# Optimization experiments

Measured on AMD Instinct MI355X. Metric: run time of the kernel, lower is better.

## Reference

```python
import jax, jax.numpy as jnp
import numpy as np
import math

B, S, D, H = 8, 256, 4096, 16
HD = D // H  # 256 == S, so the module's transposed mask application is exactly elementwise


def setup_inputs() -> dict:
    key = jax.random.key(0)
    ks = jax.random.split(key, 12)
    sc = 1.0 / math.sqrt(D)
    inp = {
        "q": jax.random.normal(ks[0], (B, S, D), dtype=jnp.float32),
        "k": jax.random.normal(ks[1], (B, S, D), dtype=jnp.float32),
        "v": jax.random.normal(ks[2], (B, S, D), dtype=jnp.float32),
        "mask": jax.random.randint(ks[3], (B, S), 0, 2),
        "Wq": jax.random.normal(ks[4], (D, D), dtype=jnp.float32) * sc,
        "bq": jnp.zeros((D,), dtype=jnp.float32),
        "Wk": jax.random.normal(ks[5], (D, D), dtype=jnp.float32) * sc,
        "bk": jnp.zeros((D,), dtype=jnp.float32),
        "Wv": jax.random.normal(ks[6], (D, D), dtype=jnp.float32) * sc,
        "bv": jnp.zeros((D,), dtype=jnp.float32),
        "Wo": jax.random.normal(ks[7], (D, D), dtype=jnp.float32) * sc,
        "bo": jnp.zeros((D,), dtype=jnp.float32),
    }
    return inp


def reference(q, k, v, mask, Wq, bq, Wk, bk, Wv, bv, Wo, bo):
    def proj(x, W, b):
        # nn.Linear: x @ W.T + b ; then [B,S,H,HD] -> [B,H,S,HD]
        return (x @ W.T + b).reshape(B, S, H, HD).transpose(0, 2, 1, 3)

    qh = proj(q, Wq, bq)
    kh = proj(k, Wk, bk)
    vh = proj(v, Wv, bv)

    # torch: attn_mask = (mask==0).view(bs,1,1,-1).repeat(1,H,HD,1) -> [B,H,HD,S]
    # then where(attn_mask, 0, q) against q of shape [B,H,S,HD] (elementwise since HD==S)
    am = jnp.broadcast_to((mask == 0)[:, None, None, :], (B, H, HD, S))
    qh = jnp.where(am, 0.0, qh)
    kh = jnp.where(am, 0.0, kh)

    scale = 1.0 / math.sqrt(HD)
    scores = jnp.einsum('bhqd,bhkd->bhqk', qh, kh) * scale
    w = jax.nn.softmax(scores, axis=-1)
    out = jnp.einsum('bhqk,bhkd->bhqd', w, vh)
    out = out.transpose(0, 2, 1, 3).reshape(B, S, D)
    out = out * (D ** -0.5)
    return out @ Wo.T + bo
```

## Files before the change

### kernel.cpp

```cpp
#include <hip/hip_runtime.h>


typedef _Float16 f16;
typedef f16 f16x8 __attribute__((ext_vector_type(8)));
typedef float f32x4 __attribute__((ext_vector_type(4)));

__device__ __forceinline__ void g2lds(const f16* g, f16* l) {
  __builtin_amdgcn_global_load_lds((const __attribute__((address_space(1))) void*)g,
                                   (__attribute__((address_space(3))) void*)l, 16, 0, 0);
}

__global__ __launch_bounds__(256) void cvt_kernel(const float* __restrict__ in,
                                                  f16* __restrict__ out, int n) {
  int i = (blockIdx.x * 256 + threadIdx.x) * 8;
  if (i >= n) return;
  float4 a = *(const float4*)(in + i);
  float4 b = *(const float4*)(in + i + 4);
  f16x8 o;
  o[0] = (f16)a.x; o[1] = (f16)a.y; o[2] = (f16)a.z; o[3] = (f16)a.w;
  o[4] = (f16)b.x; o[5] = (f16)b.y; o[6] = (f16)b.z; o[7] = (f16)b.w;
  *(f16x8*)(out + i) = o;
}

template<int EPI>
__global__ __launch_bounds__(512, 2) void gemm_dp(
    const f16* __restrict__ A, const f16* __restrict__ B,
    const float* __restrict__ bias, const int* __restrict__ mask,
    void* __restrict__ out, int M, int N, int K)
{
  __shared__ __align__(16) f16 lds[3 * 24576];
  const int tid = threadIdx.x;
  const int lane = tid & 63, wid = tid >> 6;
  const int wm = wid >> 2, wn = wid & 3;
  const int ln = lane & 15, lh = lane >> 4;
  const int bm = blockIdx.y, bn = blockIdx.x;

  const size_t Abase = (size_t)bm * 128 * K;
  const size_t Bbase = (size_t)bn * 256 * K;

  const int sr = tid >> 3;
  const int ss = (tid & 7) ^ (sr & 7);

  const int NT = K >> 6;

  f16* p0 = &lds[0];
  f16* p1 = &lds[24576];
  f16* p2 = &lds[2 * 24576];

#define STAGE(t_, bo_, part)                                                    \
  do {                                                                          \
    const int kt_ = (t_) << 6;                                                  \
    if ((part) == 0) {                                                          \
      g2lds(A + Abase + (size_t)sr * K + kt_ + ss * 8,         (bo_) + tid * 8);  \
      g2lds(B + Bbase + (size_t)sr * K + kt_ + ss * 8,         (bo_) + 8192 + tid * 8); \
      g2lds(B + Bbase + (size_t)(64 + sr) * K + kt_ + ss * 8,  (bo_) + 8192 + (512 + tid) * 8); \
    } else {                                                                    \
      g2lds(A + Abase + (size_t)(64 + sr) * K + kt_ + ss * 8,  (bo_) + (512 + tid) * 8); \
      g2lds(B + Bbase + (size_t)(128 + sr) * K + kt_ + ss * 8, (bo_) + 8192 + (1024 + tid) * 8); \
      g2lds(B + Bbase + (size_t)(192 + sr) * K + kt_ + ss * 8, (bo_) + 8192 + (1536 + tid) * 8); \
    }                                                                           \
  } while (0)

  const int lx = ln & 7;
  const int arow = (wm * 64 + ln) * 64;
  const int brow = (wn * 64 + ln) * 64;

#define LOADFRAGS(fa, fb, buf, ks)                                              \
  do {                                                                          \
    const f16* bA_ = (buf);                                                     \
    const f16* bB_ = (buf) + 8192;                                              \
    const int so_ = (((ks) * 4 + lh) ^ lx) * 8;                                 \
    _Pragma("unroll")                                                           \
    for (int mf = 0; mf < 4; ++mf)                                              \
      fa[mf] = *(const f16x8*)&bA_[arow + mf * 1024 + so_];                     \
    _Pragma("unroll")                                                           \
    for (int nf = 0; nf < 4; ++nf)                                              \
      fb[nf] = *(const f16x8*)&bB_[brow + nf * 1024 + so_];                     \
  } while (0)

#define MFMA16(fa, fb)                                                          \
  do {                                                                          \
    __builtin_amdgcn_s_setprio(1);                                              \
    _Pragma("unroll")                                                           \
    for (int mf = 0; mf < 4; ++mf)                                              \
      _Pragma("unroll")                                                         \
      for (int nf = 0; nf < 4; ++nf)                                            \
        acc[mf][nf] = __builtin_amdgcn_mfma_f32_16x16x32_f16(fa[mf], fb[nf],    \
                                                             acc[mf][nf], 0, 0, 0); \
    __builtin_amdgcn_s_setprio(0);                                              \
  } while (0)

  f32x4 acc[4][4] = {};
  f16x8 ca[4], cb[4], na[4], nb[4];

  STAGE(0, p0, 0); STAGE(0, p0, 1);
  STAGE(1, p1, 0); STAGE(1, p1, 1);
  asm volatile("s_waitcnt vmcnt(6)" ::: "memory");
  __builtin_amdgcn_s_barrier();
  asm volatile("" ::: "memory");
  LOADFRAGS(ca, cb, p0, 0);

  for (int t = 0; t < NT; ++t) {
    LOADFRAGS(na, nb, p0, 1);
    if (t + 2 < NT) { STAGE(t + 2, p2, 0); STAGE(t + 2, p2, 1); }
    MFMA16(ca, cb);

    if (t + 1 < NT) {
      if (t + 2 < NT) {
        asm volatile("s_waitcnt vmcnt(6)" ::: "memory");
      } else {
        asm volatile("s_waitcnt vmcnt(0)" ::: "memory");
      }
      __builtin_amdgcn_s_barrier();
      asm volatile("" ::: "memory");
      LOADFRAGS(ca, cb, p1, 0);
      MFMA16(na, nb);
      asm volatile("" ::: "memory");
      __builtin_amdgcn_s_barrier();
      asm volatile("" ::: "memory");
      f16* tp = p0; p0 = p1; p1 = p2; p2 = tp;
    } else {
      MFMA16(na, nb);
    }
  }
#undef STAGE
#undef LOADFRAGS
#undef MFMA16

#pragma unroll
  for (int mf = 0; mf < 4; ++mf)
#pragma unroll
    for (int nf = 0; nf < 4; ++nf)
#pragma unroll
      for (int i = 0; i < 4; ++i) {
        int R = bm * 128 + wm * 64 + mf * 16 + lh * 4 + i;
        int C = bn * 256 + wn * 64 + nf * 16 + ln;
        float v = acc[mf][nf][i];
        if (EPI == 0) {
          v += bias[C];
          v = mask[(R >> 8) * 256 + (C & 255)] ? v : 0.0f;
          ((f16*)out)[(size_t)((R >> 8) * 16 + (C >> 8)) * 65536 +
                      (size_t)(R & 255) * 256 + (C & 255)] = (f16)v;
        } else if (EPI == 1) {
          v += bias[R];
          ((f16*)out)[(size_t)(C >> 8) * 1048576 + (size_t)R * 256 + (C & 255)] = (f16)v;
        } else {
          v += bias[C];
          ((float*)out)[(size_t)R * N + C] = v;
        }
      }
}

__global__ __launch_bounds__(256) void attn_kernel(
    const f16* __restrict__ Q, const f16* __restrict__ Kt,
    const f16* __restrict__ Vt, f16* __restrict__ aout)
{
  __shared__ __align__(16) f16 tile[64 * 256];
  __shared__ __align__(16) f16 pbuf[64 * 256];
  const int tid = threadIdx.x;
  const int lane = tid & 63, w = tid >> 6;
  const int ln = lane & 15, lh = lane >> 4;
  const int bh = blockIdx.x >> 2, rb = blockIdx.x & 3;
  const int b = bh >> 4, h = bh & 15;
  const size_t hb = (size_t)bh * 65536;

  const int strow = tid >> 5;
  const int stsl  = (tid & 31) ^ (strow & 7);

  f16x8 aq[8];
  {
    const f16* qp = Q + hb + (size_t)(rb * 64 + w * 16 + ln) * 256;
#pragma unroll
    for (int ks = 0; ks < 8; ++ks)
      aq[ks] = *(const f16x8*)(qp + ks * 32 + lh * 8);
  }

  f32x4 sacc[16] = {};

  for (int kt = 0; kt < 4; ++kt) {
#pragma unroll
    for (int c = 0; c < 8; ++c) {
      int L = c * 256 + tid;
      int row = c * 8 + strow;
      g2lds(Kt + hb + (size_t)(kt * 64 + row) * 256 + stsl * 8, &tile[L * 8]);
    }
    __syncthreads();
#pragma unroll
    for (int nf = 0; nf < 4; ++nf) {
      f16x8 bf[8];
#pragma unroll
      for (int ks = 0; ks < 8; ++ks) {
        int r = nf * 16 + ln;
        int sl = (ks * 4 + lh) ^ (r & 7);
        bf[ks] = *(const f16x8*)&tile[r * 256 + sl * 8];
      }
#pragma unroll
      for (int ks = 0; ks < 8; ++ks)
        sacc[kt * 4 + nf] = __builtin_amdgcn_mfma_f32_16x16x32_f16(
            aq[ks], bf[ks], sacc[kt * 4 + nf], 0, 0, 0);
    }
    __syncthreads();
  }

  const float SC = 1.0f / 16.0f;
  float mrow[4] = {-1e30f, -1e30f, -1e30f, -1e30f};
#pragma unroll
  for (int t = 0; t < 16; ++t)
#pragma unroll
    for (int i = 0; i < 4; ++i) mrow[i] = fmaxf(mrow[i], sacc[t][i]);
#pragma unroll
  for (int i = 0; i < 4; ++i) {
    mrow[i] = fmaxf(mrow[i], __shfl_xor(mrow[i], 1));
    mrow[i] = fmaxf(mrow[i], __shfl_xor(mrow[i], 2));
    mrow[i] = fmaxf(mrow[i], __shfl_xor(mrow[i], 4));
    mrow[i] = fmaxf(mrow[i], __shfl_xor(mrow[i], 8));
  }
  float ssum[4] = {0.f, 0.f, 0.f, 0.f};
#pragma unroll
  for (int t = 0; t < 16; ++t)
#pragma unroll
    for (int i = 0; i < 4; ++i) {
      float p = __expf((sacc[t][i] - mrow[i]) * SC);
      sacc[t][i] = p;
      ssum[i] += p;
    }
#pragma unroll
  for (int i = 0; i < 4; ++i) {
    ssum[i] += __shfl_xor(ssum[i], 1);
    ssum[i] += __shfl_xor(ssum[i], 2);
    ssum[i] += __shfl_xor(ssum[i], 4);
    ssum[i] += __shfl_xor(ssum[i], 8);
  }
  float rs[4];
#pragma unroll
  for (int i = 0; i < 4; ++i) rs[i] = 1.0f / ssum[i];

#pragma unroll
  for (int t = 0; t < 16; ++t)
#pragma unroll
    for (int i = 0; i < 4; ++i) {
      int row = w * 16 + lh * 4 + i;
      int col = (t >> 2) * 64 + (t & 3) * 16 + ln;
      pbuf[row * 256 + (col ^ ((row & 7) << 3))] = (f16)(sacc[t][i] * rs[i]);
    }

  f16x8 pa[8];
  {
    int r = w * 16 + ln;
#pragma unroll
    for (int ks = 0; ks < 8; ++ks) {
      int col = ks * 32 + lh * 8;
      pa[ks] = *(const f16x8*)&pbuf[r * 256 + (col ^ ((r & 7) << 3))];
    }
  }

  for (int dt = 0; dt < 4; ++dt) {
#pragma unroll
    for (int c = 0; c < 8; ++c) {
      int L = c * 256 + tid;
      int row = c * 8 + strow;
      g2lds(Vt + hb + (size_t)(dt * 64 + row) * 256 + stsl * 8, &tile[L * 8]);
    }
    __syncthreads();
    f32x4 oacc[4] = {};
#pragma unroll
    for (int nf = 0; nf < 4; ++nf) {
      f16x8 bf[8];
#pragma unroll
      for (int ks = 0; ks < 8; ++ks) {
        int r = nf * 16 + ln;
        int sl = (ks * 4 + lh) ^ (r & 7);
        bf[ks] = *(const f16x8*)&tile[r * 256 + sl * 8];
      }
#pragma unroll
      for (int ks = 0; ks < 8; ++ks)
        oacc[nf] = __builtin_amdgcn_mfma_f32_16x16x32_f16(pa[ks], bf[ks], oacc[nf], 0, 0, 0);
    }
#pragma unroll
    for (int nf = 0; nf < 4; ++nf)
#pragma unroll
      for (int i = 0; i < 4; ++i) {
        int s = rb * 64 + w * 16 + lh * 4 + i;
        int d = dt * 64 + nf * 16 + ln;
        aout[(size_t)(b * 256 + s) * 4096 + h * 256 + d] = (f16)(oacc[nf][i] * 0.015625f);
      }
    __syncthreads();
  }
}

extern "C" void kernel_launch(void* const* d_in, const int* in_sizes, int n_in,
                              void* d_out, int out_size, void* d_ws, size_t ws_size,
                              hipStream_t stream) {
  const float* q  = (const float*)d_in[0];
  const float* k  = (const float*)d_in[1];
  const float* v  = (const float*)d_in[2];
  const int*   mk = (const int*)d_in[3];
  const float* Wq = (const float*)d_in[4];
  const float* bq = (const float*)d_in[5];
  const float* Wk = (const float*)d_in[6];
  const float* bk = (const float*)d_in[7];
  const float* Wv = (const float*)d_in[8];
  const float* bv = (const float*)d_in[9];
  const float* Wo = (const float*)d_in[10];
  const float* bo = (const float*)d_in[11];
  float* out = (float*)d_out;

  const size_t NQ = 2048ull * 4096;
  const size_t NW = 4096ull * 4096;
  f16* ws = (f16*)d_ws;
  f16* q16  = ws;
  f16* k16  = q16 + NQ;
  f16* v16  = k16 + NQ;
  f16* Wq16 = v16 + NQ;
  f16* Wk16 = Wq16 + NW;
  f16* Wv16 = Wk16 + NW;
  f16* Wo16 = Wv16 + NW;
  f16* Qbh  = Wo16 + NW;
  f16* Kbh  = Qbh + NQ;
  f16* Vt   = Kbh + NQ;
  f16* at16 = Vt + NQ;

  cvt_kernel<<<(int)(NQ / 2048), 256, 0, stream>>>(q, q16, (int)NQ);
  cvt_kernel<<<(int)(NQ / 2048), 256, 0, stream>>>(k, k16, (int)NQ);
  cvt_kernel<<<(int)(NQ / 2048), 256, 0, stream>>>(v, v16, (int)NQ);
  cvt_kernel<<<(int)(NW / 2048), 256, 0, stream>>>(Wq, Wq16, (int)NW);
  cvt_kernel<<<(int)(NW / 2048), 256, 0, stream>>>(Wk, Wk16, (int)NW);
  cvt_kernel<<<(int)(NW / 2048), 256, 0, stream>>>(Wv, Wv16, (int)NW);
  cvt_kernel<<<(int)(NW / 2048), 256, 0, stream>>>(Wo, Wo16, (int)NW);

  gemm_dp<0><<<dim3(16, 16), 512, 0, stream>>>(q16, Wq16, bq, mk, Qbh, 2048, 4096, 4096);
  gemm_dp<0><<<dim3(16, 16), 512, 0, stream>>>(k16, Wk16, bk, mk, Kbh, 2048, 4096, 4096);
  gemm_dp<1><<<dim3(8, 32), 512, 0, stream>>>(Wv16, v16, bv, nullptr, Vt, 4096, 2048, 4096);
  attn_kernel<<<512, 256, 0, stream>>>(Qbh, Kbh, Vt, at16);
  gemm_dp<2><<<dim3(16, 16), 512, 0, stream>>>(at16, Wo16, bo, nullptr, out, 2048, 4096, 4096);
}
```

Baseline: 403.0 us.

## Fuse Q/K/V projection GEMMs into one 256x256-tile grouped kernel

Replaces three separate projection GEMM launches with a single grouped kernel of 384 blocks, each computing a 256x256 output tile. It uses a double-buffered LDS pipeline split into four quarter-loads that interleave with MFMA phases and raise wave priority during the MFMA phases. Block indices are swizzled so neighbouring blocks share operand rows for L2 reuse. The goal is to cut launch overhead and the wave-quantization tail, and to double the arithmetic intensity per tile, in exchange for higher register and LDS pressure.

Result: slower. 471.4 us (+17.0%).

```diff
diff --git a/kernel.cpp b/kernel.cpp
--- a/kernel.cpp
+++ b/kernel.cpp
@@ -20,6 +20,165 @@
   o[0] = (f16)a.x; o[1] = (f16)a.y; o[2] = (f16)a.z; o[3] = (f16)a.w;
   o[4] = (f16)b.x; o[5] = (f16)b.y; o[6] = (f16)b.z; o[7] = (f16)b.w;
   *(f16x8*)(out + i) = o;
+}
+
+__global__ __launch_bounds__(512, 2) void gemm_qkv(
+    const f16* __restrict__ q16, const f16* __restrict__ k16,
+    const f16* __restrict__ v16, const f16* __restrict__ Wq,
+    const f16* __restrict__ Wk, const f16* __restrict__ Wv,
+    const float* __restrict__ bq, const float* __restrict__ bk,
+    const float* __restrict__ bv, const int* __restrict__ mask,
+    f16* __restrict__ Qbh, f16* __restrict__ Kbh, f16* __restrict__ Vt)
+{
+  __shared__ __align__(16) f16 lds[2][4][8192];
+  const int tid = threadIdx.x;
+  const int lane = tid & 63, wid = tid >> 6;
+  const int wm = wid >> 2, wn = wid & 3;
+  const int ln = lane & 15, lh = lane >> 4;
+  const int lnx = ln & 7;
+  const int K = 4096, NT = 64;
+
+  const int seg = blockIdx.x >> 7;
+  int inner = blockIdx.x & 127;
+  inner = (inner & 7) * 16 + (inner >> 3);
+
+  const f16 *A, *B;
+  const float* bias;
+  int nbm;
+  if (seg == 0)      { A = q16; B = Wq;  bias = bq; nbm = 8; }
+  else if (seg == 1) { A = k16; B = Wk;  bias = bk; nbm = 8; }
+  else               { A = Wv;  B = v16; bias = bv; nbm = 16; }
+  const int bm = inner % nbm, bn = inner / nbm;
+
+  const size_t Abase = (size_t)bm * 256 * K;
+  const size_t Bbase = (size_t)bn * 256 * K;
+
+  const int sr = tid >> 3;
+  const int ss = (tid & 7) ^ (sr & 7);
+
+#define STAGEC(tt, bb, c)                                                        \
+  do {                                                                           \
+    const f16* base_ = ((c) < 2) ? A + Abase + (size_t)((c) * 128) * K           \
+                                 : B + Bbase + (size_t)(((c) - 2) * 128) * K;    \
+    f16* dst_ = &lds[bb][c][0];                                                  \
+    g2lds(base_ + (size_t)sr * K + ((tt) << 6) + ss * 8, dst_ + tid * 8);        \
+    g2lds(base_ + (size_t)(64 + sr) * K + ((tt) << 6) + ss * 8,                  \
+          dst_ + (512 + tid) * 8);                                               \
+  } while (0)
+
+  f32x4 acc[8][4] = {};
+  f16x8 a03[4][2], a47[4][2], b01[2][2], b23[2][2];
+
+  STAGEC(0, 0, 0); STAGEC(0, 0, 1); STAGEC(0, 0, 2); STAGEC(0, 0, 3);
+  STAGEC(1, 1, 0);
+  asm volatile("s_waitcnt vmcnt(2)" ::: "memory");
+  __builtin_amdgcn_s_barrier();
+
+  for (int t = 0; t < NT; ++t) {
+    const int bb = t & 1;
+    const f16* cA = &lds[bb][wm][0];
+    const f16* cB = &lds[bb][2 + (wn >> 1)][0];
+    const int brow = (wn & 1) * 64;
+
+#pragma unroll
+    for (int m = 0; m < 4; ++m)
+#pragma unroll
+      for (int ks = 0; ks < 2; ++ks)
+        a03[m][ks] = *(const f16x8*)&cA[(m * 16 + ln) * 64 + ((ks * 4 + lh) ^ lnx) * 8];
+#pragma unroll
+    for (int n = 0; n < 2; ++n)
+#pragma unroll
+      for (int ks = 0; ks < 2; ++ks)
+        b01[n][ks] = *(const f16x8*)&cB[(brow + n * 16 + ln) * 64 + ((ks * 4 + lh) ^ lnx) * 8];
+    if (t + 1 < NT) STAGEC(t + 1, bb ^ 1, 1);
+    __builtin_amdgcn_s_barrier();
+    __builtin_amdgcn_s_setprio(1);
+#pragma unroll
+    for (int m = 0; m < 4; ++m)
+#pragma unroll
+      for (int n = 0; n < 2; ++n)
+#pragma unroll
+        for (int ks = 0; ks < 2; ++ks)
+          acc[m][n] = __builtin_amdgcn_mfma_f32_16x16x32_f16(a03[m][ks], b01[n][ks], acc[m][n], 0, 0, 0);
+    __builtin_amdgcn_s_setprio(0);
+    __builtin_amdgcn_s_barrier();
+
+#pragma unroll
+    for (int n = 0; n < 2; ++n)
+#pragma unroll
+      for (int ks = 0; ks < 2; ++ks)
+        b23[n][ks] = *(const f16x8*)&cB[(brow + 32 + n * 16 + ln) * 64 + ((ks * 4 + lh) ^ lnx) * 8];
+    if (t + 1 < NT) STAGEC(t + 1, bb ^ 1, 2);
+    __builtin_amdgcn_s_barrier();
+    __builtin_amdgcn_s_setprio(1);
+#pragma unroll
+    for (int m = 0; m < 4; ++m)
+#pragma unroll
+      for (int n = 0; n < 2; ++n)
+#pragma unroll
+        for (int ks = 0; ks < 2; ++ks)
+          acc[m][2 + n] = __builtin_amdgcn_mfma_f32_16x16x32_f16(a03[m][ks], b23[n][ks], acc[m][2 + n], 0, 0, 0);
+    __builtin_amdgcn_s_setprio(0);
+    __builtin_amdgcn_s_barrier();
+
+#pragma unroll
+    for (int m = 0; m < 4; ++m)
+#pragma unroll
+      for (int ks = 0; ks < 2; ++ks)
+        a47[m][ks] = *(const f16x8*)&cA[((64 + m * 16) + ln) * 64 + ((ks * 4 + lh) ^ lnx) * 8];
+    if (t + 1 < NT) STAGEC(t + 1, bb ^ 1, 3);
+    __builtin_amdgcn_s_barrier();
+    __builtin_amdgcn_s_setprio(1);
+#pragma unroll
+    for (int m = 0; m < 4; ++m)
+#pragma unroll
+      for (int n = 0; n < 2; ++n)
+#pragma unroll
+        for (int ks = 0; ks < 2; ++ks)
+          acc[4 + m][n] = __builtin_amdgcn_mfma_f32_16x16x32_f16(a47[m][ks], b01[n][ks], acc[4 + m][n], 0, 0, 0);
+    __builtin_amdgcn_s_setprio(0);
+    __builtin_amdgcn_s_barrier();
+
+    if (t + 2 < NT) {
+      STAGEC(t + 2, bb, 0);
+      asm volatile("s_waitcnt vmcnt(2)" ::: "memory");
+    } else {
+      asm volatile("s_waitcnt vmcnt(0)" ::: "memory");
+    }
+    __builtin_amdgcn_s_barrier();
+    __builtin_amdgcn_s_setprio(1);
+#pragma unroll
+    for (int m = 0; m < 4; ++m)
+#pragma unroll
+      for (int n = 0; n < 2; ++n)
+#pragma unroll
+        for (int ks = 0; ks < 2; ++ks)
+          acc[4 + m][2 + n] = __builtin_amdgcn_mfma_f32_16x16x32_f16(a47[m][ks], b23[n][ks], acc[4 + m][2 + n], 0, 0, 0);
+    __builtin_amdgcn_s_setprio(0);
+    __builtin_amdgcn_s_barrier();
+  }
+#undef STAGEC
+
+#pragma unroll
+  for (int mf = 0; mf < 8; ++mf)
+#pragma unroll
+    for (int nf = 0; nf < 4; ++nf)
+#pragma unroll
+      for (int i = 0; i < 4; ++i) {
+        int R = bm * 256 + wm * 128 + mf * 16 + lh * 4 + i;
+        int C = bn * 256 + wn * 64 + nf * 16 + ln;
+        float v = acc[mf][nf][i];
+        if (seg < 2) {
+          v += bias[C];
+          v = mask[(R >> 8) * 256 + (C & 255)] ? v : 0.0f;
+          f16* o = (seg == 0) ? Qbh : Kbh;
+          o[(size_t)((R >> 8) * 16 + (C >> 8)) * 65536 +
+            (size_t)(R & 255) * 256 + (C & 255)] = (f16)v;
+        } else {
+          v += bias[R];
+          Vt[(size_t)(C >> 8) * 1048576 + (size_t)R * 256 + (C & 255)] = (f16)v;
+        }
+      }
 }
 
 template<int EPI>
@@ -37,10 +196,8 @@
 
   const size_t Abase = (size_t)bm * 128 * K;
   const size_t Bbase = (size_t)bn * 256 * K;
-
   const int sr = tid >> 3;
   const int ss = (tid & 7) ^ (sr & 7);
-
   const int NT = K >> 6;
 
   f16* p0 = &lds[0];
@@ -136,18 +293,8 @@
         int R = bm * 128 + wm * 64 + mf * 16 + lh * 4 + i;
         int C = bn * 256 + wn * 64 + nf * 16 + ln;
         float v = acc[mf][nf][i];
-        if (EPI == 0) {
-          v += bias[C];
-          v = mask[(R >> 8) * 256 + (C & 255)] ? v : 0.0f;
-          ((f16*)out)[(size_t)((R >> 8) * 16 + (C >> 8)) * 65536 +
-                      (size_t)(R & 255) * 256 + (C & 255)] = (f16)v;
-        } else if (EPI == 1) {
-          v += bias[R];
-          ((f16*)out)[(size_t)(C >> 8) * 1048576 + (size_t)R * 256 + (C & 255)] = (f16)v;
-        } else {
-          v += bias[C];
-          ((float*)out)[(size_t)R * N + C] = v;
-        }
+        v += bias[C];
+        ((float*)out)[(size_t)R * N + C] = v;
       }
 }
 
@@ -328,9 +475,8 @@
   cvt_kernel<<<(int)(NW / 2048), 256, 0, stream>>>(Wv, Wv16, (int)NW);
   cvt_kernel<<<(int)(NW / 2048), 256, 0, stream>>>(Wo, Wo16, (int)NW);
 
-  gemm_dp<0><<<dim3(16, 16), 512, 0, stream>>>(q16, Wq16, bq, mk, Qbh, 2048, 4096, 4096);
-  gemm_dp<0><<<dim3(16, 16), 512, 0, stream>>>(k16, Wk16, bk, mk, Kbh, 2048, 4096, 4096);
-  gemm_dp<1><<<dim3(8, 32), 512, 0, stream>>>(Wv16, v16, bv, nullptr, Vt, 4096, 2048, 4096);
+  gemm_qkv<<<384, 512, 0, stream>>>(q16, k16, v16, Wq16, Wk16, Wv16,
+                                    bq, bk, bv, mk, Qbh, Kbh, Vt);
   attn_kernel<<<512, 256, 0, stream>>>(Qbh, Kbh, Vt, at16);
   gemm_dp<2><<<dim3(16, 16), 512, 0, stream>>>(at16, Wo16, bo, nullptr, out, 2048, 4096, 4096);
 }
```

## Switch GEMM to double-buffered LDS pipeline and batch conversion launches

Applied to the files above, without the earlier changes.

Replaces the triple-buffered, two-deep prefetch GEMM pipeline with a simpler double-buffered scheme. It issues one stage ahead, runs both k-halves of MFMAs, then waits for all loads (vmcnt(0)) at a single barrier per tile. LDS use falls from 144KB to 96KB per block, which may help the two-blocks-per-CU target. The cost is less prefetch depth, so global latency is hidden only behind one tile of compute. Separately, the seven fp32-to-fp16 conversion launches are merged into two, using blockIdx.y to pick the tensor, which cuts launch overhead.

Measured after the change: 464.8 us. 15.3% more time.

```diff
diff --git a/kernel.cpp b/kernel.cpp
--- a/kernel.cpp
+++ b/kernel.cpp
@@ -10,25 +10,48 @@
                                    (__attribute__((address_space(3))) void*)l, 16, 0, 0);
 }
 
-__global__ __launch_bounds__(256) void cvt_kernel(const float* __restrict__ in,
-                                                  f16* __restrict__ out, int n) {
-  int i = (blockIdx.x * 256 + threadIdx.x) * 8;
-  if (i >= n) return;
-  float4 a = *(const float4*)(in + i);
-  float4 b = *(const float4*)(in + i + 4);
+__device__ __forceinline__ void cvt8(const float* src, f16* dst, int i) {
+  float4 a = *(const float4*)(src + i);
+  float4 b = *(const float4*)(src + i + 4);
   f16x8 o;
   o[0] = (f16)a.x; o[1] = (f16)a.y; o[2] = (f16)a.z; o[3] = (f16)a.w;
   o[4] = (f16)b.x; o[5] = (f16)b.y; o[6] = (f16)b.z; o[7] = (f16)b.w;
-  *(f16x8*)(out + i) = o;
+  *(f16x8*)(dst + i) = o;
+}
+
+__global__ __launch_bounds__(256) void cvt_x(const float* __restrict__ q,
+                                             const float* __restrict__ k,
+                                             const float* __restrict__ v,
+                                             f16* __restrict__ oq, f16* __restrict__ ok,
+                                             f16* __restrict__ ov) {
+  const float* src; f16* dst;
+  if (blockIdx.y == 0)      { src = q; dst = oq; }
+  else if (blockIdx.y == 1) { src = k; dst = ok; }
+  else                      { src = v; dst = ov; }
+  cvt8(src, dst, (blockIdx.x * 256 + threadIdx.x) * 8);
+}
+
+__global__ __launch_bounds__(256) void cvt_w(const float* __restrict__ a,
+                                             const float* __restrict__ b,
+                                             const float* __restrict__ c,
+                                             const float* __restrict__ d,
+                                             f16* __restrict__ oa, f16* __restrict__ ob,
+                                             f16* __restrict__ oc, f16* __restrict__ od) {
+  const float* src; f16* dst;
+  if (blockIdx.y == 0)      { src = a; dst = oa; }
+  else if (blockIdx.y == 1) { src = b; dst = ob; }
+  else if (blockIdx.y == 2) { src = c; dst = oc; }
+  else                      { src = d; dst = od; }
+  cvt8(src, dst, (blockIdx.x * 256 + threadIdx.x) * 8);
 }
 
 template<int EPI>
-__global__ __launch_bounds__(512, 2) void gemm_dp(
+__global__ __launch_bounds__(512, 2) void gemm_sp(
     const f16* __restrict__ A, const f16* __restrict__ B,
     const float* __restrict__ bias, const int* __restrict__ mask,
     void* __restrict__ out, int M, int N, int K)
 {
-  __shared__ __align__(16) f16 lds[3 * 24576];
+  __shared__ __align__(16) f16 lds[2 * 24576];
   const int tid = threadIdx.x;
   const int lane = tid & 63, wid = tid >> 6;
   const int wm = wid >> 2, wn = wid & 3;
@@ -37,35 +60,29 @@
 
   const size_t Abase = (size_t)bm * 128 * K;
   const size_t Bbase = (size_t)bn * 256 * K;
-
   const int sr = tid >> 3;
   const int ss = (tid & 7) ^ (sr & 7);
-
   const int NT = K >> 6;
 
-  f16* p0 = &lds[0];
-  f16* p1 = &lds[24576];
-  f16* p2 = &lds[2 * 24576];
-
-#define STAGE(t_, bo_, part)                                                    \
+  f16* bufc = &lds[0];
+  f16* bufn = &lds[24576];
+
+#define STAGE(t_, bo_)                                                          \
   do {                                                                          \
     const int kt_ = (t_) << 6;                                                  \
-    if ((part) == 0) {                                                          \
-      g2lds(A + Abase + (size_t)sr * K + kt_ + ss * 8,         (bo_) + tid * 8);  \
-      g2lds(B + Bbase + (size_t)sr * K + kt_ + ss * 8,         (bo_) + 8192 + tid * 8); \
-      g2lds(B + Bbase + (size_t)(64 + sr) * K + kt_ + ss * 8,  (bo_) + 8192 + (512 + tid) * 8); \
-    } else {                                                                    \
-      g2lds(A + Abase + (size_t)(64 + sr) * K + kt_ + ss * 8,  (bo_) + (512 + tid) * 8); \
-      g2lds(B + Bbase + (size_t)(128 + sr) * K + kt_ + ss * 8, (bo_) + 8192 + (1024 + tid) * 8); \
-      g2lds(B + Bbase + (size_t)(192 + sr) * K + kt_ + ss * 8, (bo_) + 8192 + (1536 + tid) * 8); \
-    }                                                                           \
+    g2lds(A + Abase + (size_t)sr * K + kt_ + ss * 8,         (bo_) + tid * 8);  \
+    g2lds(A + Abase + (size_t)(64 + sr) * K + kt_ + ss * 8,  (bo_) + (512 + tid) * 8); \
+    g2lds(B + Bbase + (size_t)sr * K + kt_ + ss * 8,         (bo_) + 8192 + tid * 8); \
+    g2lds(B + Bbase + (size_t)(64 + sr) * K + kt_ + ss * 8,  (bo_) + 8192 + (512 + tid) * 8); \
+    g2lds(B + Bbase + (size_t)(128 + sr) * K + kt_ + ss * 8, (bo_) + 8192 + (1024 + tid) * 8); \
+    g2lds(B + Bbase + (size_t)(192 + sr) * K + kt_ + ss * 8, (bo_) + 8192 + (1536 + tid) * 8); \
   } while (0)
 
   const int lx = ln & 7;
   const int arow = (wm * 64 + ln) * 64;
   const int brow = (wn * 64 + ln) * 64;
 
-#define LOADFRAGS(fa, fb, buf, ks)                                              \
+#define LOADS(fa, fb, buf, ks)                                                  \
   do {                                                                          \
     const f16* bA_ = (buf);                                                     \
     const f16* bB_ = (buf) + 8192;                                              \
@@ -91,40 +108,27 @@
   } while (0)
 
   f32x4 acc[4][4] = {};
-  f16x8 ca[4], cb[4], na[4], nb[4];
-
-  STAGE(0, p0, 0); STAGE(0, p0, 1);
-  STAGE(1, p1, 0); STAGE(1, p1, 1);
-  asm volatile("s_waitcnt vmcnt(6)" ::: "memory");
+  f16x8 xa[4], xb[4], ya[4], yb[4];
+
+  STAGE(0, bufc);
+  asm volatile("s_waitcnt vmcnt(0)" ::: "memory");
   __builtin_amdgcn_s_barrier();
-  asm volatile("" ::: "memory");
-  LOADFRAGS(ca, cb, p0, 0);
+  LOADS(xa, xb, bufc, 0);
 
   for (int t = 0; t < NT; ++t) {
-    LOADFRAGS(na, nb, p0, 1);
-    if (t + 2 < NT) { STAGE(t + 2, p2, 0); STAGE(t + 2, p2, 1); }
-    MFMA16(ca, cb);
-
+    if (t + 1 < NT) STAGE(t + 1, bufn);
+    LOADS(ya, yb, bufc, 1);
+    MFMA16(xa, xb);
+    MFMA16(ya, yb);
     if (t + 1 < NT) {
-      if (t + 2 < NT) {
-        asm volatile("s_waitcnt vmcnt(6)" ::: "memory");
-      } else {
-        asm volatile("s_waitcnt vmcnt(0)" ::: "memory");
-      }
+      asm volatile("s_waitcnt vmcnt(0)" ::: "memory");
       __builtin_amdgcn_s_barrier();
-      asm volatile("" ::: "memory");
-      LOADFRAGS(ca, cb, p1, 0);
-      MFMA16(na, nb);
-      asm volatile("" ::: "memory");
-      __builtin_amdgcn_s_barrier();
-      asm volatile("" ::: "memory");
-      f16* tp = p0; p0 = p1; p1 = p2; p2 = tp;
-    } else {
-      MFMA16(na, nb);
+      LOADS(xa, xb, bufn, 0);
+      f16* tp = bufc; bufc = bufn; bufn = tp;
     }
   }
 #undef STAGE
-#undef LOADFRAGS
+#undef LOADS
 #undef MFMA16
 
 #pragma unroll
@@ -320,17 +324,12 @@
   f16* Vt   = Kbh + NQ;
   f16* at16 = Vt + NQ;
 
-  cvt_kernel<<<(int)(NQ / 2048), 256, 0, stream>>>(q, q16, (int)NQ);
-  cvt_kernel<<<(int)(NQ / 2048), 256, 0, stream>>>(k, k16, (int)NQ);
-  cvt_kernel<<<(int)(NQ / 2048), 256, 0, stream>>>(v, v16, (int)NQ);
-  cvt_kernel<<<(int)(NW / 2048), 256, 0, stream>>>(Wq, Wq16, (int)NW);
-  cvt_kernel<<<(int)(NW / 2048), 256, 0, stream>>>(Wk, Wk16, (int)NW);
-  cvt_kernel<<<(int)(NW / 2048), 256, 0, stream>>>(Wv, Wv16, (int)NW);
-  cvt_kernel<<<(int)(NW / 2048), 256, 0, stream>>>(Wo, Wo16, (int)NW);
-
-  gemm_dp<0><<<dim3(16, 16), 512, 0, stream>>>(q16, Wq16, bq, mk, Qbh, 2048, 4096, 4096);
-  gemm_dp<0><<<dim3(16, 16), 512, 0, stream>>>(k16, Wk16, bk, mk, Kbh, 2048, 4096, 4096);
-  gemm_dp<1><<<dim3(8, 32), 512, 0, stream>>>(Wv16, v16, bv, nullptr, Vt, 4096, 2048, 4096);
+  cvt_x<<<dim3(4096, 3), 256, 0, stream>>>(q, k, v, q16, k16, v16);
+  cvt_w<<<dim3(8192, 4), 256, 0, stream>>>(Wq, Wk, Wv, Wo, Wq16, Wk16, Wv16, Wo16);
+
+  gemm_sp<0><<<dim3(16, 16), 512, 0, stream>>>(q16, Wq16, bq, mk, Qbh, 2048, 4096, 4096);
+  gemm_sp<0><<<dim3(16, 16), 512, 0, stream>>>(k16, Wk16, bk, mk, Kbh, 2048, 4096, 4096);
+  gemm_sp<1><<<dim3(8, 32), 512, 0, stream>>>(Wv16, v16, bv, nullptr, Vt, 4096, 2048, 4096);
   attn_kernel<<<512, 256, 0, stream>>>(Qbh, Kbh, Vt, at16);
-  gemm_dp<2><<<dim3(16, 16), 512, 0, stream>>>(at16, Wo16, bo, nullptr, out, 2048, 4096, 4096);
-}
+  gemm_sp<2><<<dim3(16, 16), 512, 0, stream>>>(at16, Wo16, bo, nullptr, out, 2048, 4096, 4096);
+}
```
